# Performance work log

Hardware: AMD Instinct MI355X
Metric: run time of the kernel (lower is better)

The kernel has to match this reference:

```python
import jax, jax.numpy as jnp
import numpy as np

D_IN = 768
D_OUT = 768
NUM_HEADS = 12
HEAD_DIM = D_OUT // NUM_HEADS


def setup_inputs() -> dict:
    key = jax.random.key(0)
    ks = jax.random.split(key, 9)
    s = 1.0 / np.sqrt(D_IN)
    x = jax.random.normal(ks[0], (8, 1024, D_IN), dtype=jnp.float32)
    Wq = jax.random.uniform(ks[1], (D_IN, D_OUT), jnp.float32, -s, s)
    Wk = jax.random.uniform(ks[2], (D_IN, D_OUT), jnp.float32, -s, s)
    Wv = jax.random.uniform(ks[3], (D_IN, D_OUT), jnp.float32, -s, s)
    Wo = jax.random.uniform(ks[4], (D_OUT, D_OUT), jnp.float32, -s, s)
    bq = jax.random.uniform(ks[5], (D_OUT,), jnp.float32, -s, s)
    bk = jax.random.uniform(ks[6], (D_OUT,), jnp.float32, -s, s)
    bv = jax.random.uniform(ks[7], (D_OUT,), jnp.float32, -s, s)
    bo = jax.random.uniform(ks[8], (D_OUT,), jnp.float32, -s, s)
    return {"x": x, "Wq": Wq, "bq": bq, "Wk": Wk, "bk": bk,
            "Wv": Wv, "bv": bv, "Wo": Wo, "bo": bo}


def reference(x, Wq, bq, Wk, bk, Wv, bv, Wo, bo):
    b, n, _ = x.shape
    # projections -> (b, heads, n, head_dim)
    def split_heads(t):
        return t.reshape(b, n, NUM_HEADS, HEAD_DIM).transpose(0, 2, 1, 3)
    q = split_heads(x @ Wq + bq)
    k = split_heads(x @ Wk + bk)
    v = split_heads(x @ Wv + bv)
    scale = 1.0 / jnp.sqrt(jnp.float32(HEAD_DIM)).astype(x.dtype)
    scores = jnp.einsum('bhqd,bhkd->bhqk', q, k) * scale
    attn = jax.nn.softmax(scores, axis=-1)  # dropout p=0.0 -> identity
    ctx = jnp.einsum('bhqk,bhkd->bhqd', attn, v)
    ctx = ctx.transpose(0, 2, 1, 3).reshape(b, n, D_OUT)
    return ctx @ Wo + bo
```

## Files before the change

kernel.cpp:

```cpp
#include <hip/hip_runtime.h>
#include <math.h>

#define D_MODEL 768
#define NHEAD  12
#define HDIM   64
#define SEQ    1024
#define BATCH  8
#define MTOT   (BATCH*SEQ)
#define QKV_LD 2304

typedef _Float16 f16;
typedef __attribute__((ext_vector_type(2))) __fp16 fp16x2;
typedef __attribute__((ext_vector_type(4))) _Float16 f16x4;
typedef __attribute__((ext_vector_type(8))) _Float16 f16x8;
typedef __attribute__((ext_vector_type(4))) float f32x4;
typedef __attribute__((ext_vector_type(16))) float f32x16;

union PFrag { unsigned u[4]; f16x8 v; };
union PackW { fp16x2 h; unsigned u; };

__device__ inline void gload_lds16(const void* g, void* l) {
    __builtin_amdgcn_global_load_lds(
        (const __attribute__((address_space(1))) void*)g,
        (__attribute__((address_space(3))) void*)l, 16, 0, 0);
}

__global__ __launch_bounds__(256) void cvt_f32_f16(
    const float* __restrict__ in, f16* __restrict__ out, int n8)
{
    const int i = blockIdx.x * 256 + threadIdx.x;
    if (i < n8) {
        const float4 a = *(const float4*)(in + (size_t)i * 8);
        const float4 b = *(const float4*)(in + (size_t)i * 8 + 4);
        f16x8 v;
        v[0] = (f16)a.x; v[1] = (f16)a.y; v[2] = (f16)a.z; v[3] = (f16)a.w;
        v[4] = (f16)b.x; v[5] = (f16)b.y; v[6] = (f16)b.z; v[7] = (f16)b.w;
        *(f16x8*)(out + (size_t)i * 8) = v;
    }
}

__global__ __launch_bounds__(256) void concat_bias(
    const float* __restrict__ bq, const float* __restrict__ bk,
    const float* __restrict__ bv, float* __restrict__ bqkv)
{
    const int i = blockIdx.x * 256 + threadIdx.x;
    if (i < QKV_LD)
        bqkv[i] = (i < 768) ? bq[i] : (i < 1536) ? bk[i - 768] : bv[i - 1536];
}

__global__ __launch_bounds__(256) void transpose_cvt_all(
    const float* __restrict__ Wq, const float* __restrict__ Wk,
    const float* __restrict__ Wv, const float* __restrict__ Wo,
    f16* __restrict__ Wqkv_t, f16* __restrict__ Wo_t)
{
    const int z = blockIdx.z;
    const float* src = (z == 0) ? Wq : (z == 1) ? Wk : (z == 2) ? Wv : Wo;
    f16* dst = (z < 3) ? (Wqkv_t + (size_t)z * 768 * 768) : Wo_t;

    __shared__ f16 tile[64][72];
    const int t  = threadIdx.x;
    const int k0 = blockIdx.y * 64;
    const int n0 = blockIdx.x * 64;
    {
        const int r  = t >> 4;
        const int c4 = (t & 15) * 4;
        #pragma unroll
        for (int u = 0; u < 4; ++u) {
            const int row = r + u * 16;
            const float4 a = *(const float4*)&src[(size_t)(k0 + row) * 768 + n0 + c4];
            tile[row][c4 + 0] = (f16)a.x;
            tile[row][c4 + 1] = (f16)a.y;
            tile[row][c4 + 2] = (f16)a.z;
            tile[row][c4 + 3] = (f16)a.w;
        }
    }
    __syncthreads();
    {
        const int rn = t >> 3;
        const int ck = (t & 7) * 8;
        #pragma unroll
        for (int u = 0; u < 2; ++u) {
            const int n = rn + u * 32;
            f16x8 v;
            #pragma unroll
            for (int q = 0; q < 8; ++q) v[q] = tile[ck + q][n];
            *(f16x8*)&dst[(size_t)(n0 + n) * 768 + k0 + ck] = v;
        }
    }
}

template<typename OUT_T>
__global__ __launch_bounds__(256) void gemm_f16_tn(
    const f16* __restrict__ A, const f16* __restrict__ Bt,
    const float* __restrict__ bias, OUT_T* __restrict__ C,
    int M, int N, int K, int nb)
{
    __shared__ f16 As[128 * 32];
    __shared__ f16 Bs[128 * 32];

    const int t    = threadIdx.x;
    const int l    = t & 63;
    const int w    = t >> 6;
    const int l15  = l & 15;
    const int lg   = l >> 4;
    const int wrow = (w >> 1) * 64;
    const int wcol = (w & 1) * 64;

    const int orig = blockIdx.x;
    const int cpx  = gridDim.x >> 3;
    const int nid  = (orig & 7) * cpx + (orig >> 3);
    const int row0 = (nid / nb) * 128;
    const int col0 = (nid % nb) * 128;

    int src_row[2], src_koff[2], lds_off[2];
    #pragma unroll
    for (int i = 0; i < 2; ++i) {
        const int c = t + 256 * i;
        const int r = c >> 2;
        src_row[i]  = r;
        src_koff[i] = (((c & 3) - (r >> 1)) & 3) * 8;
        lds_off[i]  = c * 16;
    }

    int a_off[4], b_off[4];
    #pragma unroll
    for (int i = 0; i < 4; ++i) {
        const int ra = wrow + i * 16 + l15;
        a_off[i] = ra * 64 + (((lg + (ra >> 1)) & 3) * 16);
        const int rb = wcol + i * 16 + l15;
        b_off[i] = rb * 64 + (((lg + (rb >> 1)) & 3) * 16);
    }

    f32x4 acc[4][4];
    #pragma unroll
    for (int i = 0; i < 4; ++i)
        #pragma unroll
        for (int j = 0; j < 4; ++j)
            acc[i][j] = (f32x4){0.f, 0.f, 0.f, 0.f};

    const f16* Abase = A  + (size_t)row0 * K;
    const f16* Bbase = Bt + (size_t)col0 * K;

    for (int k0 = 0; k0 < K; k0 += 32) {
        #pragma unroll
        for (int i = 0; i < 2; ++i) {
            gload_lds16(Abase + (size_t)src_row[i] * K + k0 + src_koff[i],
                        (char*)As + lds_off[i]);
            gload_lds16(Bbase + (size_t)src_row[i] * K + k0 + src_koff[i],
                        (char*)Bs + lds_off[i]);
        }
        __syncthreads();

        f16x8 af[4], bf[4];
        #pragma unroll
        for (int i = 0; i < 4; ++i) {
            af[i] = *(const f16x8*)((const char*)As + a_off[i]);
            bf[i] = *(const f16x8*)((const char*)Bs + b_off[i]);
        }
        #pragma unroll
        for (int i = 0; i < 4; ++i)
            #pragma unroll
            for (int j = 0; j < 4; ++j)
                acc[i][j] = __builtin_amdgcn_mfma_f32_16x16x32_f16(
                    af[i], bf[j], acc[i][j], 0, 0, 0);
        __syncthreads();
    }

    #pragma unroll
    for (int j = 0; j < 4; ++j) {
        const int col = col0 + wcol + j * 16 + l15;
        const float bj = bias[col];
        #pragma unroll
        for (int i = 0; i < 4; ++i) {
            const int row = row0 + wrow + i * 16 + lg * 4;
            #pragma unroll
            for (int q = 0; q < 4; ++q)
                C[(size_t)(row + q) * N + col] = (OUT_T)(acc[i][j][q] + bj);
        }
    }
}

#define RESCALE_THR 10.0f
#define QMAP(r, hh) (((r) & 3) + 8 * ((r) >> 2) + 4 * (hh))

__global__ __launch_bounds__(256, 3) void attn_f16(
    const f16* __restrict__ QKV, f16* __restrict__ O)
{
    __shared__ f16 KsB[2][64 * 64];
    __shared__ f16 VtB[2][64 * 64];

    const int t   = threadIdx.x;
    const int w   = t >> 6;
    const int l   = t & 63;
    const int l31 = l & 31;
    const int h   = l >> 5;
    const int sl  = (l & 7) << 4;

    const int orig = blockIdx.x;
    const int s    = (orig & 7) * 96 + (orig >> 3);
    const int bh   = s >> 3;
    const int qb   = s & 7;
    const int b  = bh / NHEAD;
    const int hd = bh % NHEAD;
    const int q0 = qb * 128;

    const size_t rowbase = (size_t)b * SEQ;
    const int qcol = hd * HDIM;
    const int kcol = 768 + hd * HDIM;
    const int vcol = 1536 + hd * HDIM;

    const f16 hsc = (f16)(0.125f * 1.4426950408889634f);
    f16x8 qf[4];
    #pragma unroll
    for (int dc = 0; dc < 4; ++dc) {
        f16x8 v = *(const f16x8*)(QKV
            + (rowbase + q0 + w * 32 + l31) * QKV_LD
            + qcol + dc * 16 + h * 8);
        #pragma unroll
        for (int j = 0; j < 8; ++j) v[j] *= hsc;
        qf[dc] = v;
    }

    f32x16 ctx[2];
    #pragma unroll
    for (int dt = 0; dt < 2; ++dt)
        #pragma unroll
        for (int r = 0; r < 16; ++r) ctx[dt][r] = 0.f;
    float mrun = -INFINITY;
    float lrun = 0.f;

    const int cb  = w * 16;
    const int vk0 = (l & 15) * 4;
    const int vd0 = ((l >> 4) + 4 * w) * 4;
    const f16* kptr = QKV + (rowbase + l)   * QKV_LD + kcol + cb;
    const f16* vptr = QKV + (rowbase + vk0) * QKV_LD + vcol + vd0;
    const size_t step = (size_t)64 * QKV_LD;

    f16x8 kr0, kr1;
    f16x4 vr[4];
    kr0 = *(const f16x8*)(kptr);
    kr1 = *(const f16x8*)(kptr + 8);
    #pragma unroll
    for (int i = 0; i < 4; ++i)
        vr[i] = *(const f16x4*)(vptr + (size_t)i * QKV_LD);

    {
        char* Kd = (char*)KsB[0];
        char* Vd = (char*)VtB[0];
        *(f16x8*)(Kd + l * 128 + ((cb * 2)      ^ sl)) = kr0;
        *(f16x8*)(Kd + l * 128 + ((cb * 2 + 16) ^ sl)) = kr1;
        #pragma unroll
        for (int di = 0; di < 4; ++di) {
            f16x4 wt;
            #pragma unroll
            for (int i = 0; i < 4; ++i) wt[i] = vr[i][di];
            *(f16x4*)(Vd + (vd0 + di) * 128
                         + ((vk0 * 2) ^ (((vd0 + di) & 7) << 4))) = wt;
        }
    }
    kr0 = *(const f16x8*)(kptr + step);
    kr1 = *(const f16x8*)(kptr + step + 8);
    #pragma unroll
    for (int i = 0; i < 4; ++i)
        vr[i] = *(const f16x4*)(vptr + step + (size_t)i * QKV_LD);
    __syncthreads();

    for (int kt = 0; kt < SEQ / 64; ++kt) {
        const int p = kt & 1;
        const char* Kp = (const char*)KsB[p];
        const char* Vp = (const char*)VtB[p];

        f32x16 sacc[2];
        __builtin_amdgcn_s_setprio(1);
        #pragma unroll
        for (int kk = 0; kk < 2; ++kk) {
            f32x16 a;
            #pragma unroll
            for (int r = 0; r < 16; ++r) a[r] = 0.f;
            #pragma unroll
            for (int dc = 0; dc < 4; ++dc) {
                const f16x8 ka = *(const f16x8*)(Kp + (kk * 32 + l31) * 128
                                                    + ((dc * 32 + h * 16) ^ sl));
                a = __builtin_amdgcn_mfma_f32_32x32x16_f16(ka, qf[dc], a, 0, 0, 0);
            }
            sacc[kk] = a;
        }
        __builtin_amdgcn_s_setprio(0);

        {
            float tmax = sacc[0][0];
            #pragma unroll
            for (int r = 1; r < 16; ++r) tmax = fmaxf(tmax, sacc[0][r]);
            #pragma unroll
            for (int r = 0; r < 16; ++r) tmax = fmaxf(tmax, sacc[1][r]);
            tmax = fmaxf(tmax, __shfl_xor(tmax, 32));

            if (__any(tmax > mrun + RESCALE_THR)) {
                const float mnew = fmaxf(mrun, tmax);
                const float corr = exp2f(mrun - mnew);
                mrun = mnew;
                lrun *= corr;
                #pragma unroll
                for (int r = 0; r < 16; ++r) {
                    const float cr = __shfl(corr, QMAP(r, h));
                    ctx[0][r] *= cr;
                    ctx[1][r] *= cr;
                }
            }

            float ps = 0.f;
            #pragma unroll
            for (int kk = 0; kk < 2; ++kk)
                #pragma unroll
                for (int r = 0; r < 16; ++r) {
                    const float pe = exp2f(sacc[kk][r] - mrun);
                    ps += pe;
                    sacc[kk][r] = pe;
                }
            ps += __shfl_xor(ps, 32);
            lrun += ps;
        }

        unsigned paw[4][4];
        #pragma unroll
        for (int kk = 0; kk < 2; ++kk) {
            unsigned dw[8];
            #pragma unroll
            for (int i = 0; i < 8; ++i) {
                PackW u;
                u.h = __builtin_amdgcn_cvt_pkrtz(sacc[kk][2 * i], sacc[kk][2 * i + 1]);
                dw[i] = u.u;
            }
            const unsigned t0 = (unsigned)__shfl_xor((int)(h ? dw[0] : dw[2]), 32);
            const unsigned t1 = (unsigned)__shfl_xor((int)(h ? dw[1] : dw[3]), 32);
            const unsigned t2 = (unsigned)__shfl_xor((int)(h ? dw[4] : dw[6]), 32);
            const unsigned t3 = (unsigned)__shfl_xor((int)(h ? dw[5] : dw[7]), 32);
            paw[2 * kk][0]     = h ? t0    : dw[0];
            paw[2 * kk][1]     = h ? t1    : dw[1];
            paw[2 * kk][2]     = h ? dw[2] : t0;
            paw[2 * kk][3]     = h ? dw[3] : t1;
            paw[2 * kk + 1][0] = h ? t2    : dw[4];
            paw[2 * kk + 1][1] = h ? t3    : dw[5];
            paw[2 * kk + 1][2] = h ? dw[6] : t2;
            paw[2 * kk + 1][3] = h ? dw[7] : t3;
        }

        __builtin_amdgcn_s_setprio(1);
        #pragma unroll
        for (int c = 0; c < 4; ++c) {
            PFrag pf;
            pf.u[0] = paw[c][0]; pf.u[1] = paw[c][1];
            pf.u[2] = paw[c][2]; pf.u[3] = paw[c][3];
            #pragma unroll
            for (int dt = 0; dt < 2; ++dt) {
                const f16x8 vb = *(const f16x8*)(Vp + (dt * 32 + l31) * 128
                                                    + ((c * 32 + h * 16) ^ sl));
                ctx[dt] = __builtin_amdgcn_mfma_f32_32x32x16_f16(pf.v, vb, ctx[dt], 0, 0, 0);
            }
        }
        __builtin_amdgcn_s_setprio(0);

        if (kt < SEQ / 64 - 1) {
            char* Kd = (char*)KsB[p ^ 1];
            char* Vd = (char*)VtB[p ^ 1];
            *(f16x8*)(Kd + l * 128 + ((cb * 2)      ^ sl)) = kr0;
            *(f16x8*)(Kd + l * 128 + ((cb * 2 + 16) ^ sl)) = kr1;
            #pragma unroll
            for (int di = 0; di < 4; ++di) {
                f16x4 wt;
                #pragma unroll
                for (int i = 0; i < 4; ++i) wt[i] = vr[i][di];
                *(f16x4*)(Vd + (vd0 + di) * 128
                             + ((vk0 * 2) ^ (((vd0 + di) & 7) << 4))) = wt;
            }
            if (kt < SEQ / 64 - 2) {
                const f16* kp = kptr + (size_t)(kt + 2) * step;
                const f16* vp = vptr + (size_t)(kt + 2) * step;
                kr0 = *(const f16x8*)(kp);
                kr1 = *(const f16x8*)(kp + 8);
                #pragma unroll
                for (int i = 0; i < 4; ++i)
                    vr[i] = *(const f16x4*)(vp + (size_t)i * QKV_LD);
            }
        }
        __syncthreads();
    }

    {
        const float inv = 1.0f / lrun;
        #pragma unroll
        for (int r = 0; r < 16; ++r) {
            const float iv = __shfl(inv, QMAP(r, h));
            const size_t row = rowbase + q0 + w * 32 + QMAP(r, h);
            O[row * D_MODEL + qcol + l31]      = (f16)(ctx[0][r] * iv);
            O[row * D_MODEL + qcol + 32 + l31] = (f16)(ctx[1][r] * iv);
        }
    }
}

extern "C" void kernel_launch(void* const* d_in, const int* in_sizes, int n_in,
                              void* d_out, int out_size, void* d_ws, size_t ws_size,
                              hipStream_t stream) {
    const float* x  = (const float*)d_in[0];
    const float* Wq = (const float*)d_in[1];
    const float* bq = (const float*)d_in[2];
    const float* Wk = (const float*)d_in[3];
    const float* bk = (const float*)d_in[4];
    const float* Wv = (const float*)d_in[5];
    const float* bv = (const float*)d_in[6];
    const float* Wo = (const float*)d_in[7];
    const float* bo = (const float*)d_in[8];
    float* out = (float*)d_out;

    char* ws = (char*)d_ws;
    f16*   QKV     = (f16*)(ws);
    f16*   xh      = (f16*)(ws + 37748736);
    f16*   ctxh    = (f16*)(ws + 37748736 + 12582912);
    f16*   Wqkv_t  = (f16*)(ws + 37748736 + 2 * 12582912);
    f16*   Wo_t    = (f16*)(ws + 37748736 + 2 * 12582912 + 3538944);
    float* bqkv    = (float*)(ws + 37748736 + 2 * 12582912 + 3538944 + 1179648);

    hipLaunchKernelGGL(cvt_f32_f16, dim3(MTOT * D_MODEL / 8 / 256), dim3(256), 0, stream,
                       x, xh, MTOT * D_MODEL / 8);
    hipLaunchKernelGGL(concat_bias, dim3(9), dim3(256), 0, stream, bq, bk, bv, bqkv);
    hipLaunchKernelGGL(transpose_cvt_all, dim3(12, 12, 4), dim3(256), 0, stream,
                       Wq, Wk, Wv, Wo, Wqkv_t, Wo_t);

    hipLaunchKernelGGL((gemm_f16_tn<f16>), dim3((QKV_LD / 128) * (MTOT / 128)), dim3(256), 0, stream,
                       xh, Wqkv_t, bqkv, QKV, MTOT, QKV_LD, D_MODEL, QKV_LD / 128);

    hipLaunchKernelGGL(attn_f16, dim3((SEQ / 128) * BATCH * NHEAD), dim3(256), 0, stream,
                       QKV, ctxh);

    hipLaunchKernelGGL((gemm_f16_tn<float>), dim3((D_MODEL / 128) * (MTOT / 128)), dim3(256), 0, stream,
                       ctxh, Wo_t, bo, out, MTOT, D_MODEL, D_MODEL, D_MODEL / 128);
}
```

Before: 139.8 us.

## Deepen GEMM K-tile, fuse bias concat into convert, reorder attention PV MFMA

Doubles the GEMM K-step from 32 to 64 with a matching 8-way swizzled LDS layout, halving the number of barrier pairs per output tile at the cost of double the shared memory per block. Folds the bias concatenation into the x conversion kernel to save one launch. In attention, moves the P·V MFMA block after the LDS stores and global prefetch of the next K/V tile so the memory traffic is issued earlier and can overlap the matrix work.

```diff
diff --git a/kernel.cpp b/kernel.cpp
--- a/kernel.cpp
+++ b/kernel.cpp
@@ -25,8 +25,10 @@
         (__attribute__((address_space(3))) void*)l, 16, 0, 0);
 }
 
-__global__ __launch_bounds__(256) void cvt_f32_f16(
-    const float* __restrict__ in, f16* __restrict__ out, int n8)
+__global__ __launch_bounds__(256) void cvt_f32_f16_fused(
+    const float* __restrict__ in, f16* __restrict__ out, int n8,
+    const float* __restrict__ bq, const float* __restrict__ bk,
+    const float* __restrict__ bv, float* __restrict__ bqkv)
 {
     const int i = blockIdx.x * 256 + threadIdx.x;
     if (i < n8) {
@@ -37,13 +39,6 @@
         v[4] = (f16)b.x; v[5] = (f16)b.y; v[6] = (f16)b.z; v[7] = (f16)b.w;
         *(f16x8*)(out + (size_t)i * 8) = v;
     }
-}
-
-__global__ __launch_bounds__(256) void concat_bias(
-    const float* __restrict__ bq, const float* __restrict__ bk,
-    const float* __restrict__ bv, float* __restrict__ bqkv)
-{
-    const int i = blockIdx.x * 256 + threadIdx.x;
     if (i < QKV_LD)
         bqkv[i] = (i < 768) ? bq[i] : (i < 1536) ? bk[i - 768] : bv[i - 1536];
 }
@@ -95,14 +90,13 @@
     const float* __restrict__ bias, OUT_T* __restrict__ C,
     int M, int N, int K, int nb)
 {
-    __shared__ f16 As[128 * 32];
-    __shared__ f16 Bs[128 * 32];
+    __shared__ f16 As[128 * 64];
+    __shared__ f16 Bs[128 * 64];
 
     const int t    = threadIdx.x;
-    const int l    = t & 63;
+    const int l15  = (t & 63) & 15;
+    const int lg   = (t & 63) >> 4;
     const int w    = t >> 6;
-    const int l15  = l & 15;
-    const int lg   = l >> 4;
     const int wrow = (w >> 1) * 64;
     const int wcol = (w & 1) * 64;
 
@@ -112,23 +106,26 @@
     const int row0 = (nid / nb) * 128;
     const int col0 = (nid % nb) * 128;
 
-    int src_row[2], src_koff[2], lds_off[2];
-    #pragma unroll
-    for (int i = 0; i < 2; ++i) {
+    int src_row[4], src_koff[4], lds_off[4];
+    #pragma unroll
+    for (int i = 0; i < 4; ++i) {
         const int c = t + 256 * i;
-        const int r = c >> 2;
+        const int r = c >> 3;
         src_row[i]  = r;
-        src_koff[i] = (((c & 3) - (r >> 1)) & 3) * 8;
+        src_koff[i] = ((((c & 7) - (r >> 1)) & 7)) * 8;
         lds_off[i]  = c * 16;
     }
 
-    int a_off[4], b_off[4];
+    int a_off[4][2], b_off[4][2];
     #pragma unroll
     for (int i = 0; i < 4; ++i) {
         const int ra = wrow + i * 16 + l15;
-        a_off[i] = ra * 64 + (((lg + (ra >> 1)) & 3) * 16);
         const int rb = wcol + i * 16 + l15;
-        b_off[i] = rb * 64 + (((lg + (rb >> 1)) & 3) * 16);
+        #pragma unroll
+        for (int s = 0; s < 2; ++s) {
+            a_off[i][s] = ra * 128 + (((s * 4 + lg + (ra >> 1)) & 7) * 16);
+            b_off[i][s] = rb * 128 + (((s * 4 + lg + (rb >> 1)) & 7) * 16);
+        }
     }
 
     f32x4 acc[4][4];
@@ -141,9 +138,9 @@
     const f16* Abase = A  + (size_t)row0 * K;
     const f16* Bbase = Bt + (size_t)col0 * K;
 
-    for (int k0 = 0; k0 < K; k0 += 32) {
-        #pragma unroll
-        for (int i = 0; i < 2; ++i) {
+    for (int k0 = 0; k0 < K; k0 += 64) {
+        #pragma unroll
+        for (int i = 0; i < 4; ++i) {
             gload_lds16(Abase + (size_t)src_row[i] * K + k0 + src_koff[i],
                         (char*)As + lds_off[i]);
             gload_lds16(Bbase + (size_t)src_row[i] * K + k0 + src_koff[i],
@@ -151,18 +148,21 @@
         }
         __syncthreads();
 
-        f16x8 af[4], bf[4];
-        #pragma unroll
-        for (int i = 0; i < 4; ++i) {
-            af[i] = *(const f16x8*)((const char*)As + a_off[i]);
-            bf[i] = *(const f16x8*)((const char*)Bs + b_off[i]);
-        }
-        #pragma unroll
-        for (int i = 0; i < 4; ++i)
-            #pragma unroll
-            for (int j = 0; j < 4; ++j)
-                acc[i][j] = __builtin_amdgcn_mfma_f32_16x16x32_f16(
-                    af[i], bf[j], acc[i][j], 0, 0, 0);
+        #pragma unroll
+        for (int s = 0; s < 2; ++s) {
+            f16x8 af[4], bf[4];
+            #pragma unroll
+            for (int i = 0; i < 4; ++i) {
+                af[i] = *(const f16x8*)((const char*)As + a_off[i][s]);
+                bf[i] = *(const f16x8*)((const char*)Bs + b_off[i][s]);
+            }
+            #pragma unroll
+            for (int i = 0; i < 4; ++i)
+                #pragma unroll
+                for (int j = 0; j < 4; ++j)
+                    acc[i][j] = __builtin_amdgcn_mfma_f32_16x16x32_f16(
+                        af[i], bf[j], acc[i][j], 0, 0, 0);
+        }
         __syncthreads();
     }
 
@@ -345,21 +345,6 @@
             paw[2 * kk + 1][3] = h ? dw[7] : t3;
         }
 
-        __builtin_amdgcn_s_setprio(1);
-        #pragma unroll
-        for (int c = 0; c < 4; ++c) {
-            PFrag pf;
-            pf.u[0] = paw[c][0]; pf.u[1] = paw[c][1];
-            pf.u[2] = paw[c][2]; pf.u[3] = paw[c][3];
-            #pragma unroll
-            for (int dt = 0; dt < 2; ++dt) {
-                const f16x8 vb = *(const f16x8*)(Vp + (dt * 32 + l31) * 128
-                                                    + ((c * 32 + h * 16) ^ sl));
-                ctx[dt] = __builtin_amdgcn_mfma_f32_32x32x16_f16(pf.v, vb, ctx[dt], 0, 0, 0);
-            }
-        }
-        __builtin_amdgcn_s_setprio(0);
-
         if (kt < SEQ / 64 - 1) {
             char* Kd = (char*)KsB[p ^ 1];
             char* Vd = (char*)VtB[p ^ 1];
@@ -383,6 +368,22 @@
                     vr[i] = *(const f16x4*)(vp + (size_t)i * QKV_LD);
             }
         }
+
+        __builtin_amdgcn_s_setprio(1);
+        #pragma unroll
+        for (int c = 0; c < 4; ++c) {
+            PFrag pf;
+            pf.u[0] = paw[c][0]; pf.u[1] = paw[c][1];
+            pf.u[2] = paw[c][2]; pf.u[3] = paw[c][3];
+            #pragma unroll
+            for (int dt = 0; dt < 2; ++dt) {
+                const f16x8 vb = *(const f16x8*)(Vp + (dt * 32 + l31) * 128
+                                                    + ((c * 32 + h * 16) ^ sl));
+                ctx[dt] = __builtin_amdgcn_mfma_f32_32x32x16_f16(pf.v, vb, ctx[dt], 0, 0, 0);
+            }
+        }
+        __builtin_amdgcn_s_setprio(0);
+
         __syncthreads();
     }
 
@@ -420,9 +421,8 @@
     f16*   Wo_t    = (f16*)(ws + 37748736 + 2 * 12582912 + 3538944);
     float* bqkv    = (float*)(ws + 37748736 + 2 * 12582912 + 3538944 + 1179648);
 
-    hipLaunchKernelGGL(cvt_f32_f16, dim3(MTOT * D_MODEL / 8 / 256), dim3(256), 0, stream,
-                       x, xh, MTOT * D_MODEL / 8);
-    hipLaunchKernelGGL(concat_bias, dim3(9), dim3(256), 0, stream, bq, bk, bv, bqkv);
+    hipLaunchKernelGGL(cvt_f32_f16_fused, dim3(MTOT * D_MODEL / 8 / 256), dim3(256), 0, stream,
+                       x, xh, MTOT * D_MODEL / 8, bq, bk, bv, bqkv);
     hipLaunchKernelGGL(transpose_cvt_all, dim3(12, 12, 4), dim3(256), 0, stream,
                        Wq, Wk, Wv, Wo, Wqkv_t, Wo_t);
 
```

Result: no change. 139.7 us (-0.1%).
